# Kernel tuning notes

Measured on AMD Instinct MI355X. Metric: run time of the kernel, lower is better.

## Reference

```python
import jax, jax.numpy as jnp
import numpy as np

N = 100000
IN_DIM, HID_DIM, EMB_DIM = 128, 64, 32
E = 1600000


def _gcn_conv(x, W, b, src, tgt, n):
    """PyG GCNConv: linear transform, add self-loops, sym-normalized scatter-add.
    W: [in, out], b: [out]. src/tgt: [E'] incl. self-loops handled by caller."""
    h = x @ W  # [n, out] -- transform before propagate (PyG order)
    deg = jax.ops.segment_sum(jnp.ones_like(tgt, dtype=h.dtype), tgt, num_segments=n)
    dinv = jnp.where(deg > 0, jax.lax.rsqrt(deg), 0.0)
    norm = dinv[src] * dinv[tgt]  # [E']
    msgs = h[src] * norm[:, None]  # [E', out]
    out = jax.ops.segment_sum(msgs, tgt, num_segments=n)
    return out + b


def setup_inputs() -> dict:
    key = jax.random.key(0)
    ks = jax.random.split(key, 6)
    x = jax.random.normal(ks[0], (N, IN_DIM), dtype=jnp.float32)
    edge_index = jax.random.randint(ks[1], (2, E), 0, N, dtype=jnp.int64)
    s1 = 1.0 / np.sqrt(IN_DIM)
    s2 = 1.0 / np.sqrt(HID_DIM)
    W1 = jax.random.uniform(ks[2], (IN_DIM, HID_DIM), jnp.float32, -s1, s1)
    b1 = jnp.zeros((HID_DIM,), jnp.float32)
    W2 = jax.random.uniform(ks[3], (HID_DIM, EMB_DIM), jnp.float32, -s2, s2)
    b2 = jnp.zeros((EMB_DIM,), jnp.float32)
    return {"x": x, "W1": W1, "b1": b1, "W2": W2, "b2": b2, "edge_index": edge_index}


def reference(x, W1, b1, W2, b2, edge_index):
    n = x.shape[0]
    src, tgt = edge_index[0], edge_index[1]
    # add self-loops once (same graph used by both convs)
    loops = jnp.arange(n, dtype=edge_index.dtype)
    src_sl = jnp.concatenate([src, loops])
    tgt_sl = jnp.concatenate([tgt, loops])
    h = jax.nn.relu(_gcn_conv(x, W1, b1, src_sl, tgt_sl, n))
    z = _gcn_conv(h, W2, b2, src_sl, tgt_sl, n)  # [n, EMB_DIM]
    # decode on original edges: edge-wise dot product
    recon = jnp.sum(z[src] * z[tgt], axis=1)  # [E]
    return z, recon
```

## Files before the change

kernel.cpp:

```cpp
#include <hip/hip_runtime.h>
#include <hip/hip_fp16.h>
#include <math.h>


#define NBMAX 512
#define BSHIFT 8
#define BNODES 256
#define CH 16384
#define PTH 512
#define CAPSHIFT 13
#define CAP (1 << CAPSHIFT)

typedef _Float16 half8 __attribute__((ext_vector_type(8)));
typedef float floatx4 __attribute__((ext_vector_type(4)));

static inline int divup(int a, int b) { return (a + b - 1) / b; }

__device__ inline void acc8(__half2* a, float4 v) {
    const __half2* h = (const __half2*)&v;
    a[0] = __hadd2(a[0], h[0]);
    a[1] = __hadd2(a[1], h[1]);
    a[2] = __hadd2(a[2], h[2]);
    a[3] = __hadd2(a[3], h[3]);
}
__device__ inline unsigned short f2bf(float f) {
    unsigned u = __builtin_bit_cast(unsigned, f);
    u = (u + 0x7FFFu + ((u >> 16) & 1u)) >> 16;
    return (unsigned short)u;
}


__global__ void k_init(int* __restrict__ gcur, unsigned* __restrict__ hs_pad,
                       unsigned* __restrict__ zs_pad) {
    int t = threadIdx.x;
    for (int b = t; b < NBMAX; b += 256) gcur[b] = b << CAPSHIFT;
    if (t < 32) hs_pad[t] = 0;
    else if (t < 48) zs_pad[t - 32] = 0;
}


__global__ __launch_bounds__(PTH) void k_part(const int* __restrict__ src,
                                              const int* __restrict__ tgt,
                                              int* __restrict__ gcur,
                                              unsigned* __restrict__ ebuf, int E, int NB) {
    __shared__ int h[NBMAX];
    __shared__ int base[NBMAX];
    int tid = threadIdx.x;
    int e0 = blockIdx.x * CH;
    for (int b = tid; b < NB; b += PTH) h[b] = 0;
    __syncthreads();
#pragma unroll
    for (int r = 0; r < 8; r++) {
        int e = e0 + (r * PTH + tid) * 4;
        if (e + 3 < E) {
            int4 t4 = *(const int4*)(tgt + e);
            atomicAdd(&h[t4.x >> BSHIFT], 1);
            atomicAdd(&h[t4.y >> BSHIFT], 1);
            atomicAdd(&h[t4.z >> BSHIFT], 1);
            atomicAdd(&h[t4.w >> BSHIFT], 1);
        } else {
            for (int j = 0; j < 4; j++) {
                int ee = e + j;
                if (ee < E) atomicAdd(&h[tgt[ee] >> BSHIFT], 1);
            }
        }
    }
    __syncthreads();
    for (int b = tid; b < NB; b += PTH) {
        int c = h[b];
        base[b] = c ? atomicAdd(&gcur[b], c) : 0;
    }
    __syncthreads();
#pragma unroll
    for (int r = 0; r < 8; r++) {
        int e = e0 + (r * PTH + tid) * 4;
        if (e + 3 < E) {
            int4 t4 = *(const int4*)(tgt + e);
            int4 s4 = *(const int4*)(src + e);
            int tv[4] = {t4.x, t4.y, t4.z, t4.w};
            int sw[4] = {s4.x, s4.y, s4.z, s4.w};
#pragma unroll
            for (int j = 0; j < 4; j++) {
                int t = tv[j];
                int pos = atomicAdd(&base[t >> BSHIFT], 1);
                ebuf[pos] = ((unsigned)(t & (BNODES - 1)) << 23) | (unsigned)sw[j];
            }
        } else {
            for (int j = 0; j < 4; j++) {
                int ee = e + j;
                if (ee < E) {
                    int t = tgt[ee];
                    int pos = atomicAdd(&base[t >> BSHIFT], 1);
                    ebuf[pos] = ((unsigned)(t & (BNODES - 1)) << 23) | (unsigned)src[ee];
                }
            }
        }
    }
}


__global__ __launch_bounds__(256) void k_bfill(const unsigned* __restrict__ ebuf,
                                               const int* __restrict__ gcur,
                                               int* __restrict__ rowbeg,
                                               int* __restrict__ rowend,
                                               int* __restrict__ col,
                                               float* __restrict__ dinv, int n) {
    __shared__ int s_cnt[BNODES];
    __shared__ int s_scan[BNODES];
    __shared__ int s_cur[BNODES];
    int b = blockIdx.x, tid = threadIdx.x;
    int nbase = b << BSHIFT;
    int ebase = b << CAPSHIFT;
    int eend = gcur[b];
    s_cnt[tid] = 0;
    __syncthreads();
    for (int e = ebase + tid; e < eend; e += BNODES) {
        atomicAdd(&s_cnt[ebuf[e] >> 23], 1);
    }
    __syncthreads();
    s_scan[tid] = s_cnt[tid];
    __syncthreads();
    for (int off = 1; off < BNODES; off <<= 1) {
        int t = (tid >= off) ? s_scan[tid - off] : 0;
        __syncthreads();
        s_scan[tid] += t;
        __syncthreads();
    }
    int excl = s_scan[tid] - s_cnt[tid];
    s_cur[tid] = excl;
    int node = nbase + tid;
    if (node < n) {
        rowbeg[node] = ebase + excl;
        rowend[node] = ebase + excl + s_cnt[tid];
        dinv[node] = rsqrtf((float)(s_cnt[tid] + 1));
    }
    __syncthreads();
    for (int e = ebase + tid; e < eend; e += BNODES) {
        unsigned p = ebuf[e];
        int pos = atomicAdd(&s_cur[p >> 23], 1);
        col[ebase + pos] = (int)(p & 0x7FFFFFu);
    }
}


__global__ __launch_bounds__(512) void k_mm1(const float* __restrict__ x,
                                             const float* __restrict__ W1,
                                             const float* __restrict__ dinv,
                                             __half* __restrict__ hs, int n) {
    __shared__ _Float16 Wt[64 * 136];
    int tid = threadIdx.x;
    int nbase = blockIdx.x * 128;
#pragma unroll
    for (int i = 0; i < 8; i++) {
        int f = tid + i * 512;
        int c = f & 63, kp = f >> 6;
        float a = W1[(size_t)(2 * kp) * 64 + c];
        float b = W1[(size_t)(2 * kp + 1) * 64 + c];
        *(__half2*)&Wt[c * 136 + 2 * kp] = __floats2half2_rn(a, b);
    }
    __syncthreads();
    int w = tid >> 6, lane = tid & 63;
    int quad = lane >> 4, m = lane & 15;
    int arow = nbase + w * 16 + m;
    const float* xb = x + (size_t)min(arow, n - 1) * 128;
    floatx4 acc[4] = {{0.f, 0.f, 0.f, 0.f}, {0.f, 0.f, 0.f, 0.f},
                      {0.f, 0.f, 0.f, 0.f}, {0.f, 0.f, 0.f, 0.f}};
#pragma unroll
    for (int kt = 0; kt < 4; kt++) {
        float4 v0 = *(const float4*)(xb + kt * 32 + quad * 8);
        float4 v1 = *(const float4*)(xb + kt * 32 + quad * 8 + 4);
        union { half8 h8; __half2 h2[4]; } ua;
        ua.h2[0] = __floats2half2_rn(v0.x, v0.y);
        ua.h2[1] = __floats2half2_rn(v0.z, v0.w);
        ua.h2[2] = __floats2half2_rn(v1.x, v1.y);
        ua.h2[3] = __floats2half2_rn(v1.z, v1.w);
#pragma unroll
        for (int ct = 0; ct < 4; ct++) {
            half8 b = *(const half8*)&Wt[(ct * 16 + m) * 136 + kt * 32 + quad * 8];
            acc[ct] = __builtin_amdgcn_mfma_f32_16x16x32_f16(ua.h8, b, acc[ct], 0, 0, 0);
        }
    }
#pragma unroll
    for (int reg = 0; reg < 4; reg++) {
        int node = nbase + w * 16 + quad * 4 + reg;
        if (node < n) {
            float d = dinv[node];
#pragma unroll
            for (int ct = 0; ct < 4; ct++) {
                hs[(size_t)node * 64 + ct * 16 + m] = __float2half(acc[ct][reg] * d);
            }
        }
    }
}


__global__ __launch_bounds__(256) void k_conv1(const __half* __restrict__ hs,
                                               const int* __restrict__ rowbeg,
                                               const int* __restrict__ rowend,
                                               const int* __restrict__ col,
                                               const float* __restrict__ dinv,
                                               const float* __restrict__ b1,
                                               __half* __restrict__ h2, int n) {
    int gw = (blockIdx.x * 256 + threadIdx.x) >> 6;
    int lane = threadIdx.x & 63;
    int q = lane >> 4, ln = lane & 15;
    int w = gw * 4 + q;
    if (w >= n) return;
    int qb = q << 4;
    int el = ln >> 3, fl = ln & 7;
    int beg = rowbeg[w], end = rowend[w];
    int deg = end - beg;
    int m = min(16, deg);
    int m2 = min(16, deg - 16);
    int sl = (ln < m) ? col[beg + ln] : 0;
    int sl2 = (ln < m2) ? col[beg + 16 + ln] : 0;
    __half2 a2[4];
#pragma unroll
    for (int j = 0; j < 4; j++) a2[j] = __half2half2(__float2half(0.f));
    int rs = (el == 0) ? w : n;
    float4 S = *(const float4*)(hs + (size_t)rs * 64 + fl * 8);
    float4 L[4];
#pragma unroll
    for (int r = 0; r < 4; r++) {
        int idx = 2 * r + el;
        int s = __shfl(sl, qb + idx);
        int a = (idx < m) ? s : n;
        L[r] = *(const float4*)(hs + (size_t)a * 64 + fl * 8);
    }
    acc8(a2, S);
#pragma unroll
    for (int r = 0; r < 4; r++) acc8(a2, L[r]);
#pragma unroll
    for (int r = 0; r < 4; r++) {
        int idx = 8 + 2 * r + el;
        int s = __shfl(sl, qb + idx);
        int a = (idx < m) ? s : n;
        L[r] = *(const float4*)(hs + (size_t)a * 64 + fl * 8);
    }
#pragma unroll
    for (int r = 0; r < 4; r++) acc8(a2, L[r]);
    if (deg > 16) {
#pragma unroll
        for (int r = 0; r < 4; r++) {
            int idx = 2 * r + el;
            int s = __shfl(sl2, qb + idx);
            int a = (idx < m2) ? s : n;
            L[r] = *(const float4*)(hs + (size_t)a * 64 + fl * 8);
        }
#pragma unroll
        for (int r = 0; r < 4; r++) acc8(a2, L[r]);
#pragma unroll
        for (int r = 0; r < 4; r++) {
            int idx = 8 + 2 * r + el;
            int s = __shfl(sl2, qb + idx);
            int a = (idx < m2) ? s : n;
            L[r] = *(const float4*)(hs + (size_t)a * 64 + fl * 8);
        }
#pragma unroll
        for (int r = 0; r < 4; r++) acc8(a2, L[r]);
    }
    if (deg > 32) {
        for (int b0 = 32; b0 < deg; b0 += 16) {
            int mc = min(16, deg - b0);
            int sl3 = (ln < mc) ? col[beg + b0 + ln] : 0;
            for (int r = 0; r < 8; r++) {
                int idx = 2 * r + el;
                int s = __shfl(sl3, qb + idx);
                int a = (idx < mc) ? s : n;
                float4 v = *(const float4*)(hs + (size_t)a * 64 + fl * 8);
                acc8(a2, v);
            }
        }
    }
    float r[8];
#pragma unroll
    for (int j = 0; j < 4; j++) {
        float2 f = __half22float2(a2[j]);
        r[2 * j] = f.x;
        r[2 * j + 1] = f.y;
    }
#pragma unroll
    for (int j = 0; j < 8; j++) r[j] += __shfl_xor(r[j], 8);

    if (el == 0) {
        float d = dinv[w];
        float4 bb0 = *(const float4*)(b1 + fl * 8);
        float4 bb1 = *(const float4*)(b1 + fl * 8 + 4);
        union { float4 f; __half2 h[4]; } u;
        u.h[0] = __floats2half2_rn(fmaxf(r[0] * d + bb0.x, 0.f),
                                   fmaxf(r[1] * d + bb0.y, 0.f));
        u.h[1] = __floats2half2_rn(fmaxf(r[2] * d + bb0.z, 0.f),
                                   fmaxf(r[3] * d + bb0.w, 0.f));
        u.h[2] = __floats2half2_rn(fmaxf(r[4] * d + bb1.x, 0.f),
                                   fmaxf(r[5] * d + bb1.y, 0.f));
        u.h[3] = __floats2half2_rn(fmaxf(r[6] * d + bb1.z, 0.f),
                                   fmaxf(r[7] * d + bb1.w, 0.f));
        *(float4*)(h2 + (size_t)w * 64 + fl * 8) = u.f;
    }
}


__global__ __launch_bounds__(256) void k_mm2(const __half* __restrict__ h2,
                                             const float* __restrict__ W2,
                                             const float* __restrict__ dinv,
                                             __half* __restrict__ zs, int n) {
    __shared__ _Float16 Wt[32 * 72];
    int tid = threadIdx.x;
    int nbase = blockIdx.x * 64;
#pragma unroll
    for (int i = 0; i < 4; i++) {
        int f = tid + i * 256;
        int c = f & 31, kp = f >> 5;
        float a = W2[(size_t)(2 * kp) * 32 + c];
        float b = W2[(size_t)(2 * kp + 1) * 32 + c];
        *(__half2*)&Wt[c * 72 + 2 * kp] = __floats2half2_rn(a, b);
    }
    __syncthreads();
    int w = tid >> 6, lane = tid & 63;
    int quad = lane >> 4, m = lane & 15;
    int arow = nbase + w * 16 + m;
    const __half* abase = h2 + (size_t)min(arow, n - 1) * 64;
    floatx4 acc[2] = {{0.f, 0.f, 0.f, 0.f}, {0.f, 0.f, 0.f, 0.f}};
#pragma unroll
    for (int kt = 0; kt < 2; kt++) {
        half8 a = *(const half8*)(abase + kt * 32 + quad * 8);
#pragma unroll
        for (int ct = 0; ct < 2; ct++) {
            half8 b = *(const half8*)&Wt[(ct * 16 + m) * 72 + kt * 32 + quad * 8];
            acc[ct] = __builtin_amdgcn_mfma_f32_16x16x32_f16(a, b, acc[ct], 0, 0, 0);
        }
    }
#pragma unroll
    for (int reg = 0; reg < 4; reg++) {
        int node = nbase + w * 16 + quad * 4 + reg;
        if (node < n) {
            float d = dinv[node];
#pragma unroll
            for (int ct = 0; ct < 2; ct++) {
                zs[(size_t)node * 32 + ct * 16 + m] = __float2half(acc[ct][reg] * d);
            }
        }
    }
}


__global__ __launch_bounds__(256) void k_conv2(const __half* __restrict__ zs,
                                               const int* __restrict__ rowbeg,
                                               const int* __restrict__ rowend,
                                               const int* __restrict__ col,
                                               const float* __restrict__ dinv,
                                               const float* __restrict__ b2,
                                               float* __restrict__ zout,
                                               unsigned short* __restrict__ zh, int n) {
    int gw = (blockIdx.x * 256 + threadIdx.x) >> 6;
    int lane = threadIdx.x & 63;
    int q = lane >> 4, ln = lane & 15;
    int w = gw * 4 + q;
    if (w >= n) return;
    int qb = q << 4;
    int el = ln >> 2, fl = ln & 3;
    int beg = rowbeg[w], end = rowend[w];
    int deg = end - beg;
    int m = min(16, deg);
    int m2 = min(16, deg - 16);
    int sl = (ln < m) ? col[beg + ln] : 0;
    int sl2 = (ln < m2) ? col[beg + 16 + ln] : 0;
    __half2 a2[4];
#pragma unroll
    for (int j = 0; j < 4; j++) a2[j] = __half2half2(__float2half(0.f));
    int rs = (el == 0) ? w : n;
    float4 S = *(const float4*)(zs + (size_t)rs * 32 + fl * 8);
    float4 L[4];
#pragma unroll
    for (int r = 0; r < 4; r++) {
        int idx = 4 * r + el;
        int s = __shfl(sl, qb + idx);
        int a = (idx < m) ? s : n;
        L[r] = *(const float4*)(zs + (size_t)a * 32 + fl * 8);
    }
    acc8(a2, S);
#pragma unroll
    for (int r = 0; r < 4; r++) acc8(a2, L[r]);
    if (deg > 16) {
#pragma unroll
        for (int r = 0; r < 4; r++) {
            int idx = 4 * r + el;
            int s = __shfl(sl2, qb + idx);
            int a = (idx < m2) ? s : n;
            L[r] = *(const float4*)(zs + (size_t)a * 32 + fl * 8);
        }
#pragma unroll
        for (int r = 0; r < 4; r++) acc8(a2, L[r]);
    }
    if (deg > 32) {
        for (int b0 = 32; b0 < deg; b0 += 16) {
            int mc = min(16, deg - b0);
            int sl3 = (ln < mc) ? col[beg + b0 + ln] : 0;
            for (int r = 0; r < 4; r++) {
                int idx = 4 * r + el;
                int s = __shfl(sl3, qb + idx);
                int a = (idx < mc) ? s : n;
                float4 v = *(const float4*)(zs + (size_t)a * 32 + fl * 8);
                acc8(a2, v);
            }
        }
    }
    float r[8];
#pragma unroll
    for (int j = 0; j < 4; j++) {
        float2 f = __half22float2(a2[j]);
        r[2 * j] = f.x;
        r[2 * j + 1] = f.y;
    }
#pragma unroll
    for (int d = 4; d < 16; d <<= 1)
#pragma unroll
        for (int j = 0; j < 8; j++) r[j] += __shfl_xor(r[j], d);

    if (el == 0) {
        float d = dinv[w];
        float4 bb0 = *(const float4*)(b2 + fl * 8);
        float4 bb1 = *(const float4*)(b2 + fl * 8 + 4);
        float o0 = r[0] * d + bb0.x, o1 = r[1] * d + bb0.y;
        float o2 = r[2] * d + bb0.z, o3 = r[3] * d + bb0.w;
        float o4 = r[4] * d + bb1.x, o5 = r[5] * d + bb1.y;
        float o6 = r[6] * d + bb1.z, o7 = r[7] * d + bb1.w;
        *(float4*)(zout + (size_t)w * 32 + fl * 8) = make_float4(o0, o1, o2, o3);
        *(float4*)(zout + (size_t)w * 32 + fl * 8 + 4) = make_float4(o4, o5, o6, o7);
        uint4 p;
        p.x = (unsigned)f2bf(o0) | ((unsigned)f2bf(o1) << 16);
        p.y = (unsigned)f2bf(o2) | ((unsigned)f2bf(o3) << 16);
        p.z = (unsigned)f2bf(o4) | ((unsigned)f2bf(o5) << 16);
        p.w = (unsigned)f2bf(o6) | ((unsigned)f2bf(o7) << 16);
        *(uint4*)(zh + (size_t)w * 32 + fl * 8) = p;
    }
}


__device__ inline float bfdot8(uint4 a, uint4 b) {
    const unsigned* pa = (const unsigned*)&a;
    const unsigned* pb = (const unsigned*)&b;
    float v = 0.f;
#pragma unroll
    for (int w = 0; w < 4; w++) {
        float alo = __builtin_bit_cast(float, pa[w] << 16);
        float ahi = __builtin_bit_cast(float, pa[w] & 0xFFFF0000u);
        float blo = __builtin_bit_cast(float, pb[w] << 16);
        float bhi = __builtin_bit_cast(float, pb[w] & 0xFFFF0000u);
        v += alo * blo + ahi * bhi;
    }
    return v;
}

__global__ __launch_bounds__(256) void k_decode(const unsigned short* __restrict__ zh,
                                                const int* __restrict__ src,
                                                const int* __restrict__ tgt,
                                                float* __restrict__ recon, int E) {
    int g = (blockIdx.x * 256 + threadIdx.x) >> 2;
    int fl = threadIdx.x & 3;
    int e0 = g * 4;
    if (e0 >= E) return;
    int cnt = min(4, E - e0);
    int s[4], t[4];
#pragma unroll
    for (int q = 0; q < 4; q++) {
        int e = (q < cnt) ? e0 + q : e0;
        s[q] = src[e];
        t[q] = tgt[e];
    }
    uint4 Za[4], Zb[4];
#pragma unroll
    for (int q = 0; q < 4; q++) {
        Za[q] = *(const uint4*)(zh + (size_t)s[q] * 32 + fl * 8);
        Zb[q] = *(const uint4*)(zh + (size_t)t[q] * 32 + fl * 8);
    }
    float v[4];
#pragma unroll
    for (int q = 0; q < 4; q++) {
        float x = bfdot8(Za[q], Zb[q]);
        x += __shfl_xor(x, 1);
        x += __shfl_xor(x, 2);
        v[q] = x;
    }
    if (fl == 0) {
        if (cnt == 4) {
            *(float4*)(recon + e0) = make_float4(v[0], v[1], v[2], v[3]);
        } else {
            for (int q = 0; q < cnt; q++) recon[e0 + q] = v[q];
        }
    }
}

extern "C" void kernel_launch(void* const* d_in, const int* in_sizes, int n_in,
                              void* d_out, int out_size, void* d_ws, size_t ws_size,
                              hipStream_t stream) {
    const float* x = (const float*)d_in[0];
    const float* W1 = (const float*)d_in[1];
    const float* b1 = (const float*)d_in[2];
    const float* W2 = (const float*)d_in[3];
    const float* b2 = (const float*)d_in[4];
    const int* ei = (const int*)d_in[5];

    int N = in_sizes[0] / 128;
    int E = in_sizes[5] / 2;
    const int* src = ei;
    const int* tgt = ei + E;
    int NB = divup(N, BNODES);

    char* ws = (char*)d_ws;
    size_t off = 0;
    auto alloc = [&](size_t bytes) {
        size_t r = off;
        off += (bytes + 255) & ~(size_t)255;
        return r;
    };
    int* gcur = (int*)(ws + alloc(NBMAX * 4));
    unsigned* ebuf = (unsigned*)(ws + alloc((size_t)NB * CAP * 4));
    int* col = (int*)(ws + alloc((size_t)NB * CAP * 4));
    int* rowbeg = (int*)(ws + alloc((size_t)N * 4));
    int* rowend = (int*)(ws + alloc((size_t)N * 4));
    float* dinv = (float*)(ws + alloc((size_t)N * 4));
    __half* hs = (__half*)(ws + alloc((size_t)(N + 1) * 64 * 2));
    __half* h2 = (__half*)(ws + alloc((size_t)N * 64 * 2));
    __half* zs = (__half*)(ws + alloc((size_t)(N + 1) * 32 * 2));
    unsigned short* zh = (unsigned short*)(ws + alloc((size_t)N * 32 * 2));

    float* zout = (float*)d_out;
    float* recon = zout + (size_t)N * 32;

    k_init<<<1, 256, 0, stream>>>(gcur, (unsigned*)(hs + (size_t)N * 64),
                                  (unsigned*)(zs + (size_t)N * 32));
    k_part<<<divup(E, CH), PTH, 0, stream>>>(src, tgt, gcur, ebuf, E, NB);
    k_bfill<<<NB, BNODES, 0, stream>>>(ebuf, gcur, rowbeg, rowend, col, dinv, N);

    k_mm1<<<divup(N, 128), 512, 0, stream>>>(x, W1, dinv, hs, N);
    k_conv1<<<divup(N, 16), 256, 0, stream>>>(hs, rowbeg, rowend, col, dinv, b1, h2, N);
    k_mm2<<<divup(N, 64), 256, 0, stream>>>(h2, W2, dinv, zs, N);
    k_conv2<<<divup(N, 16), 256, 0, stream>>>(zs, rowbeg, rowend, col, dinv, b2, zout, zh, N);
    k_decode<<<divup(E, 256), 256, 0, stream>>>(zh, src, tgt, recon, E);
}
```

Measured before the change: 226.2 us.

## Fuse all GCN stages into one persistent cooperative kernel with grid syncs

```diff
diff --git a/kernel.cpp b/kernel.cpp
--- a/kernel.cpp
+++ b/kernel.cpp
@@ -1,13 +1,15 @@
 #include <hip/hip_runtime.h>
+#include <hip/hip_cooperative_groups.h>
 #include <hip/hip_fp16.h>
 #include <math.h>
+
+namespace cg = cooperative_groups;
 
 
 #define NBMAX 512
 #define BSHIFT 8
 #define BNODES 256
-#define CH 16384
-#define PTH 512
+#define CHF 16384
 #define CAPSHIFT 13
 #define CAP (1 << CAPSHIFT)
 
@@ -28,6 +30,460 @@
     u = (u + 0x7FFFu + ((u >> 16) & 1u)) >> 16;
     return (unsigned short)u;
 }
+__device__ inline float bfdot8(uint4 a, uint4 b) {
+    const unsigned* pa = (const unsigned*)&a;
+    const unsigned* pb = (const unsigned*)&b;
+    float v = 0.f;
+#pragma unroll
+    for (int w = 0; w < 4; w++) {
+        float alo = __builtin_bit_cast(float, pa[w] << 16);
+        float ahi = __builtin_bit_cast(float, pa[w] & 0xFFFF0000u);
+        float blo = __builtin_bit_cast(float, pb[w] << 16);
+        float bhi = __builtin_bit_cast(float, pb[w] & 0xFFFF0000u);
+        v += alo * blo + ahi * bhi;
+    }
+    return v;
+}
+
+
+struct GP {
+    const float* x; const float* W1; const float* b1;
+    const float* W2; const float* b2;
+    const int* src; const int* tgt;
+    int* gcur; unsigned* ebuf; int* col; int* rowbeg; int* rowend; float* dinv;
+    __half* hs; __half* h2; __half* zs; unsigned short* zh;
+    float* zout; float* recon;
+    int n, e, nb, npart;
+};
+
+__global__ __launch_bounds__(256) void k_fused(GP p) {
+    cg::grid_group grid = cg::this_grid();
+    __shared__ union {
+        struct { int h[NBMAX]; int base[NBMAX]; } pt;
+        struct { int cnt[BNODES]; int scan[BNODES]; int cur[BNODES]; } bf;
+        _Float16 wt1[64 * 136];
+        _Float16 wt2[32 * 72];
+    } sm;
+    const int tid = threadIdx.x;
+    const int nblk = gridDim.x;
+
+    if (blockIdx.x == 0) {
+        for (int b = tid; b < NBMAX; b += 256) p.gcur[b] = b << CAPSHIFT;
+        unsigned* hp = (unsigned*)(p.hs + (size_t)p.n * 64);
+        unsigned* zp = (unsigned*)(p.zs + (size_t)p.n * 32);
+        if (tid < 32) hp[tid] = 0;
+        else if (tid < 48) zp[tid - 32] = 0;
+    }
+    grid.sync();
+
+    for (int vb = blockIdx.x; vb < p.npart; vb += nblk) {
+        __syncthreads();
+        int e0 = vb * CHF;
+        for (int b = tid; b < p.nb; b += 256) sm.pt.h[b] = 0;
+        __syncthreads();
+        for (int r = 0; r < 16; r++) {
+            int e = e0 + (r * 256 + tid) * 4;
+            if (e + 3 < p.e) {
+                int4 t4 = *(const int4*)(p.tgt + e);
+                atomicAdd(&sm.pt.h[t4.x >> BSHIFT], 1);
+                atomicAdd(&sm.pt.h[t4.y >> BSHIFT], 1);
+                atomicAdd(&sm.pt.h[t4.z >> BSHIFT], 1);
+                atomicAdd(&sm.pt.h[t4.w >> BSHIFT], 1);
+            } else {
+                for (int j = 0; j < 4; j++) {
+                    int ee = e + j;
+                    if (ee < p.e) atomicAdd(&sm.pt.h[p.tgt[ee] >> BSHIFT], 1);
+                }
+            }
+        }
+        __syncthreads();
+        for (int b = tid; b < p.nb; b += 256) {
+            int c = sm.pt.h[b];
+            sm.pt.base[b] = c ? atomicAdd(&p.gcur[b], c) : 0;
+        }
+        __syncthreads();
+        for (int r = 0; r < 16; r++) {
+            int e = e0 + (r * 256 + tid) * 4;
+            if (e + 3 < p.e) {
+                int4 t4 = *(const int4*)(p.tgt + e);
+                int4 s4 = *(const int4*)(p.src + e);
+                int tv[4] = {t4.x, t4.y, t4.z, t4.w};
+                int sw[4] = {s4.x, s4.y, s4.z, s4.w};
+#pragma unroll
+                for (int j = 0; j < 4; j++) {
+                    int t = tv[j];
+                    int pos = atomicAdd(&sm.pt.base[t >> BSHIFT], 1);
+                    p.ebuf[pos] = ((unsigned)(t & (BNODES - 1)) << 23) | (unsigned)sw[j];
+                }
+            } else {
+                for (int j = 0; j < 4; j++) {
+                    int ee = e + j;
+                    if (ee < p.e) {
+                        int t = p.tgt[ee];
+                        int pos = atomicAdd(&sm.pt.base[t >> BSHIFT], 1);
+                        p.ebuf[pos] = ((unsigned)(t & (BNODES - 1)) << 23) | (unsigned)p.src[ee];
+                    }
+                }
+            }
+        }
+    }
+    grid.sync();
+
+    for (int vb = blockIdx.x; vb < p.nb; vb += nblk) {
+        __syncthreads();
+        int nbase = vb << BSHIFT;
+        int ebase = vb << CAPSHIFT;
+        int eend = p.gcur[vb];
+        sm.bf.cnt[tid] = 0;
+        __syncthreads();
+        for (int e = ebase + tid; e < eend; e += BNODES) {
+            atomicAdd(&sm.bf.cnt[p.ebuf[e] >> 23], 1);
+        }
+        __syncthreads();
+        sm.bf.scan[tid] = sm.bf.cnt[tid];
+        __syncthreads();
+        for (int off = 1; off < BNODES; off <<= 1) {
+            int t = (tid >= off) ? sm.bf.scan[tid - off] : 0;
+            __syncthreads();
+            sm.bf.scan[tid] += t;
+            __syncthreads();
+        }
+        int excl = sm.bf.scan[tid] - sm.bf.cnt[tid];
+        sm.bf.cur[tid] = excl;
+        int node = nbase + tid;
+        if (node < p.n) {
+            p.rowbeg[node] = ebase + excl;
+            p.rowend[node] = ebase + excl + sm.bf.cnt[tid];
+            p.dinv[node] = rsqrtf((float)(sm.bf.cnt[tid] + 1));
+        }
+        __syncthreads();
+        for (int e = ebase + tid; e < eend; e += BNODES) {
+            unsigned q = p.ebuf[e];
+            int pos = atomicAdd(&sm.bf.cur[q >> 23], 1);
+            p.col[ebase + pos] = (int)(q & 0x7FFFFFu);
+        }
+    }
+    grid.sync();
+
+    {
+#pragma unroll
+        for (int i = 0; i < 16; i++) {
+            int f = tid + i * 256;
+            int c = f & 63, kp = f >> 6;
+            float a = p.W1[(size_t)(2 * kp) * 64 + c];
+            float b = p.W1[(size_t)(2 * kp + 1) * 64 + c];
+            *(__half2*)&sm.wt1[c * 136 + 2 * kp] = __floats2half2_rn(a, b);
+        }
+        __syncthreads();
+        int w = tid >> 6, lane = tid & 63;
+        int quad = lane >> 4, m = lane & 15;
+        int ntile = (p.n + 63) >> 6;
+        for (int vt = blockIdx.x; vt < ntile; vt += nblk) {
+            int nbase = vt * 64;
+            int arow = nbase + w * 16 + m;
+            const float* xb = p.x + (size_t)(arow < p.n ? arow : p.n - 1) * 128;
+            floatx4 acc[4] = {{0.f, 0.f, 0.f, 0.f}, {0.f, 0.f, 0.f, 0.f},
+                              {0.f, 0.f, 0.f, 0.f}, {0.f, 0.f, 0.f, 0.f}};
+#pragma unroll
+            for (int kt = 0; kt < 4; kt++) {
+                float4 v0 = *(const float4*)(xb + kt * 32 + quad * 8);
+                float4 v1 = *(const float4*)(xb + kt * 32 + quad * 8 + 4);
+                union { half8 h8; __half2 h2[4]; } ua;
+                ua.h2[0] = __floats2half2_rn(v0.x, v0.y);
+                ua.h2[1] = __floats2half2_rn(v0.z, v0.w);
+                ua.h2[2] = __floats2half2_rn(v1.x, v1.y);
+                ua.h2[3] = __floats2half2_rn(v1.z, v1.w);
+#pragma unroll
+                for (int ct = 0; ct < 4; ct++) {
+                    half8 b = *(const half8*)&sm.wt1[(ct * 16 + m) * 136 + kt * 32 + quad * 8];
+                    acc[ct] = __builtin_amdgcn_mfma_f32_16x16x32_f16(ua.h8, b, acc[ct], 0, 0, 0);
+                }
+            }
+#pragma unroll
+            for (int reg = 0; reg < 4; reg++) {
+                int node = nbase + w * 16 + quad * 4 + reg;
+                if (node < p.n) {
+                    float d = p.dinv[node];
+#pragma unroll
+                    for (int ct = 0; ct < 4; ct++) {
+                        p.hs[(size_t)node * 64 + ct * 16 + m] = __float2half(acc[ct][reg] * d);
+                    }
+                }
+            }
+        }
+    }
+    grid.sync();
+
+    {
+        int wid = (blockIdx.x * 256 + tid) >> 6;
+        int wstride = (nblk * 256) >> 6;
+        int lane = tid & 63;
+        int q = lane >> 4, ln = lane & 15, qb = q << 4;
+        int el = ln >> 3, fl = ln & 7;
+        for (int gw = wid; gw * 4 < p.n; gw += wstride) {
+            int w = gw * 4 + q;
+            if (w < p.n) {
+                int beg = p.rowbeg[w], end = p.rowend[w];
+                int deg = end - beg;
+                int m = min(16, deg);
+                int m2 = min(16, deg - 16);
+                int sl = (ln < m) ? p.col[beg + ln] : 0;
+                int sl2 = (ln < m2) ? p.col[beg + 16 + ln] : 0;
+                __half2 a2[4];
+#pragma unroll
+                for (int j = 0; j < 4; j++) a2[j] = __half2half2(__float2half(0.f));
+                int rs = (el == 0) ? w : p.n;
+                float4 S = *(const float4*)(p.hs + (size_t)rs * 64 + fl * 8);
+                float4 L[4];
+#pragma unroll
+                for (int r = 0; r < 4; r++) {
+                    int idx = 2 * r + el;
+                    int s = __shfl(sl, qb + idx);
+                    int a = (idx < m) ? s : p.n;
+                    L[r] = *(const float4*)(p.hs + (size_t)a * 64 + fl * 8);
+                }
+                acc8(a2, S);
+#pragma unroll
+                for (int r = 0; r < 4; r++) acc8(a2, L[r]);
+#pragma unroll
+                for (int r = 0; r < 4; r++) {
+                    int idx = 8 + 2 * r + el;
+                    int s = __shfl(sl, qb + idx);
+                    int a = (idx < m) ? s : p.n;
+                    L[r] = *(const float4*)(p.hs + (size_t)a * 64 + fl * 8);
+                }
+#pragma unroll
+                for (int r = 0; r < 4; r++) acc8(a2, L[r]);
+                if (deg > 16) {
+#pragma unroll
+                    for (int r = 0; r < 4; r++) {
+                        int idx = 2 * r + el;
+                        int s = __shfl(sl2, qb + idx);
+                        int a = (idx < m2) ? s : p.n;
+                        L[r] = *(const float4*)(p.hs + (size_t)a * 64 + fl * 8);
+                    }
+#pragma unroll
+                    for (int r = 0; r < 4; r++) acc8(a2, L[r]);
+#pragma unroll
+                    for (int r = 0; r < 4; r++) {
+                        int idx = 8 + 2 * r + el;
+                        int s = __shfl(sl2, qb + idx);
+                        int a = (idx < m2) ? s : p.n;
+                        L[r] = *(const float4*)(p.hs + (size_t)a * 64 + fl * 8);
+                    }
+#pragma unroll
+                    for (int r = 0; r < 4; r++) acc8(a2, L[r]);
+                }
+                if (deg > 32) {
+                    for (int b0 = 32; b0 < deg; b0 += 16) {
+                        int mc = min(16, deg - b0);
+                        int sl3 = (ln < mc) ? p.col[beg + b0 + ln] : 0;
+                        for (int r = 0; r < 8; r++) {
+                            int idx = 2 * r + el;
+                            int s = __shfl(sl3, qb + idx);
+                            int a = (idx < mc) ? s : p.n;
+                            float4 v = *(const float4*)(p.hs + (size_t)a * 64 + fl * 8);
+                            acc8(a2, v);
+                        }
+                    }
+                }
+                float r[8];
+#pragma unroll
+                for (int j = 0; j < 4; j++) {
+                    float2 f = __half22float2(a2[j]);
+                    r[2 * j] = f.x;
+                    r[2 * j + 1] = f.y;
+                }
+#pragma unroll
+                for (int j = 0; j < 8; j++) r[j] += __shfl_xor(r[j], 8);
+                if (el == 0) {
+                    float d = p.dinv[w];
+                    float4 bb0 = *(const float4*)(p.b1 + fl * 8);
+                    float4 bb1 = *(const float4*)(p.b1 + fl * 8 + 4);
+                    union { float4 f; __half2 h[4]; } u;
+                    u.h[0] = __floats2half2_rn(fmaxf(r[0] * d + bb0.x, 0.f),
+                                               fmaxf(r[1] * d + bb0.y, 0.f));
+                    u.h[1] = __floats2half2_rn(fmaxf(r[2] * d + bb0.z, 0.f),
+                                               fmaxf(r[3] * d + bb0.w, 0.f));
+                    u.h[2] = __floats2half2_rn(fmaxf(r[4] * d + bb1.x, 0.f),
+                                               fmaxf(r[5] * d + bb1.y, 0.f));
+                    u.h[3] = __floats2half2_rn(fmaxf(r[6] * d + bb1.z, 0.f),
+                                               fmaxf(r[7] * d + bb1.w, 0.f));
+                    *(float4*)(p.h2 + (size_t)w * 64 + fl * 8) = u.f;
+                }
+            }
+        }
+    }
+    grid.sync();
+
+    {
+#pragma unroll
+        for (int i = 0; i < 4; i++) {
+            int f = tid + i * 256;
+            int c = f & 31, kp = f >> 5;
+            float a = p.W2[(size_t)(2 * kp) * 32 + c];
+            float b = p.W2[(size_t)(2 * kp + 1) * 32 + c];
+            *(__half2*)&sm.wt2[c * 72 + 2 * kp] = __floats2half2_rn(a, b);
+        }
+        __syncthreads();
+        int w = tid >> 6, lane = tid & 63;
+        int quad = lane >> 4, m = lane & 15;
+        int ntile = (p.n + 63) >> 6;
+        for (int vt = blockIdx.x; vt < ntile; vt += nblk) {
+            int nbase = vt * 64;
+            int arow = nbase + w * 16 + m;
+            const __half* abase = p.h2 + (size_t)(arow < p.n ? arow : p.n - 1) * 64;
+            floatx4 acc[2] = {{0.f, 0.f, 0.f, 0.f}, {0.f, 0.f, 0.f, 0.f}};
+#pragma unroll
+            for (int kt = 0; kt < 2; kt++) {
+                half8 a = *(const half8*)(abase + kt * 32 + quad * 8);
+#pragma unroll
+                for (int ct = 0; ct < 2; ct++) {
+                    half8 b = *(const half8*)&sm.wt2[(ct * 16 + m) * 72 + kt * 32 + quad * 8];
+                    acc[ct] = __builtin_amdgcn_mfma_f32_16x16x32_f16(a, b, acc[ct], 0, 0, 0);
+                }
+            }
+#pragma unroll
+            for (int reg = 0; reg < 4; reg++) {
+                int node = nbase + w * 16 + quad * 4 + reg;
+                if (node < p.n) {
+                    float d = p.dinv[node];
+#pragma unroll
+                    for (int ct = 0; ct < 2; ct++) {
+                        p.zs[(size_t)node * 32 + ct * 16 + m] = __float2half(acc[ct][reg] * d);
+                    }
+                }
+            }
+        }
+    }
+    grid.sync();
+
+    {
+        int wid = (blockIdx.x * 256 + tid) >> 6;
+        int wstride = (nblk * 256) >> 6;
+        int lane = tid & 63;
+        int q = lane >> 4, ln = lane & 15, qb = q << 4;
+        int el = ln >> 2, fl = ln & 3;
+        for (int gw = wid; gw * 4 < p.n; gw += wstride) {
+            int w = gw * 4 + q;
+            if (w < p.n) {
+                int beg = p.rowbeg[w], end = p.rowend[w];
+                int deg = end - beg;
+                int m = min(16, deg);
+                int m2 = min(16, deg - 16);
+                int sl = (ln < m) ? p.col[beg + ln] : 0;
+                int sl2 = (ln < m2) ? p.col[beg + 16 + ln] : 0;
+                __half2 a2[4];
+#pragma unroll
+                for (int j = 0; j < 4; j++) a2[j] = __half2half2(__float2half(0.f));
+                int rs = (el == 0) ? w : p.n;
+                float4 S = *(const float4*)(p.zs + (size_t)rs * 32 + fl * 8);
+                float4 L[4];
+#pragma unroll
+                for (int r = 0; r < 4; r++) {
+                    int idx = 4 * r + el;
+                    int s = __shfl(sl, qb + idx);
+                    int a = (idx < m) ? s : p.n;
+                    L[r] = *(const float4*)(p.zs + (size_t)a * 32 + fl * 8);
+                }
+                acc8(a2, S);
+#pragma unroll
+                for (int r = 0; r < 4; r++) acc8(a2, L[r]);
+                if (deg > 16) {
+#pragma unroll
+                    for (int r = 0; r < 4; r++) {
+                        int idx = 4 * r + el;
+                        int s = __shfl(sl2, qb + idx);
+                        int a = (idx < m2) ? s : p.n;
+                        L[r] = *(const float4*)(p.zs + (size_t)a * 32 + fl * 8);
+                    }
+#pragma unroll
+                    for (int r = 0; r < 4; r++) acc8(a2, L[r]);
+                }
+                if (deg > 32) {
+                    for (int b0 = 32; b0 < deg; b0 += 16) {
+                        int mc = min(16, deg - b0);
+                        int sl3 = (ln < mc) ? p.col[beg + b0 + ln] : 0;
+                        for (int r = 0; r < 4; r++) {
+                            int idx = 4 * r + el;
+                            int s = __shfl(sl3, qb + idx);
+                            int a = (idx < mc) ? s : p.n;
+                            float4 v = *(const float4*)(p.zs + (size_t)a * 32 + fl * 8);
+                            acc8(a2, v);
+                        }
+                    }
+                }
+                float r[8];
+#pragma unroll
+                for (int j = 0; j < 4; j++) {
+                    float2 f = __half22float2(a2[j]);
+                    r[2 * j] = f.x;
+                    r[2 * j + 1] = f.y;
+                }
+#pragma unroll
+                for (int d = 4; d < 16; d <<= 1)
+#pragma unroll
+                    for (int j = 0; j < 8; j++) r[j] += __shfl_xor(r[j], d);
+                if (el == 0) {
+                    float d = p.dinv[w];
+                    float4 bb0 = *(const float4*)(p.b2 + fl * 8);
+                    float4 bb1 = *(const float4*)(p.b2 + fl * 8 + 4);
+                    float o0 = r[0] * d + bb0.x, o1 = r[1] * d + bb0.y;
+                    float o2 = r[2] * d + bb0.z, o3 = r[3] * d + bb0.w;
+                    float o4 = r[4] * d + bb1.x, o5 = r[5] * d + bb1.y;
+                    float o6 = r[6] * d + bb1.z, o7 = r[7] * d + bb1.w;
+                    *(float4*)(p.zout + (size_t)w * 32 + fl * 8) = make_float4(o0, o1, o2, o3);
+                    *(float4*)(p.zout + (size_t)w * 32 + fl * 8 + 4) = make_float4(o4, o5, o6, o7);
+                    uint4 pk;
+                    pk.x = (unsigned)f2bf(o0) | ((unsigned)f2bf(o1) << 16);
+                    pk.y = (unsigned)f2bf(o2) | ((unsigned)f2bf(o3) << 16);
+                    pk.z = (unsigned)f2bf(o4) | ((unsigned)f2bf(o5) << 16);
+                    pk.w = (unsigned)f2bf(o6) | ((unsigned)f2bf(o7) << 16);
+                    *(uint4*)(p.zh + (size_t)w * 32 + fl * 8) = pk;
+                }
+            }
+        }
+    }
+    grid.sync();
+
+    {
+        int g = (blockIdx.x * 256 + tid) >> 2;
+        int gstride = nblk * 64;
+        int fl = tid & 3;
+        for (; g * 4 < p.e; g += gstride) {
+            int e0 = g * 4;
+            int cnt = min(4, p.e - e0);
+            int s[4], t[4];
+#pragma unroll
+            for (int q = 0; q < 4; q++) {
+                int e = (q < cnt) ? e0 + q : e0;
+                s[q] = p.src[e];
+                t[q] = p.tgt[e];
+            }
+            uint4 Za[4], Zb[4];
+#pragma unroll
+            for (int q = 0; q < 4; q++) {
+                Za[q] = *(const uint4*)(p.zh + (size_t)s[q] * 32 + fl * 8);
+                Zb[q] = *(const uint4*)(p.zh + (size_t)t[q] * 32 + fl * 8);
+            }
+            float v[4];
+#pragma unroll
+            for (int q = 0; q < 4; q++) {
+                float xv = bfdot8(Za[q], Zb[q]);
+                xv += __shfl_xor(xv, 1);
+                xv += __shfl_xor(xv, 2);
+                v[q] = xv;
+            }
+            if (fl == 0) {
+                if (cnt == 4) {
+                    *(float4*)(p.recon + e0) = make_float4(v[0], v[1], v[2], v[3]);
+                } else {
+                    for (int q = 0; q < cnt; q++) p.recon[e0 + q] = v[q];
+                }
+            }
+        }
+    }
+}
 
 
 __global__ void k_init(int* __restrict__ gcur, unsigned* __restrict__ hs_pad,
@@ -38,20 +494,19 @@
     else if (t < 48) zs_pad[t - 32] = 0;
 }
 
-
-__global__ __launch_bounds__(PTH) void k_part(const int* __restrict__ src,
+__global__ __launch_bounds__(512) void k_part(const int* __restrict__ src,
                                               const int* __restrict__ tgt,
                                               int* __restrict__ gcur,
                                               unsigned* __restrict__ ebuf, int E, int NB) {
     __shared__ int h[NBMAX];
     __shared__ int base[NBMAX];
     int tid = threadIdx.x;
-    int e0 = blockIdx.x * CH;
-    for (int b = tid; b < NB; b += PTH) h[b] = 0;
+    int e0 = blockIdx.x * CHF;
+    for (int b = tid; b < NB; b += 512) h[b] = 0;
     __syncthreads();
 #pragma unroll
     for (int r = 0; r < 8; r++) {
-        int e = e0 + (r * PTH + tid) * 4;
+        int e = e0 + (r * 512 + tid) * 4;
         if (e + 3 < E) {
             int4 t4 = *(const int4*)(tgt + e);
             atomicAdd(&h[t4.x >> BSHIFT], 1);
@@ -66,14 +521,14 @@
         }
     }
     __syncthreads();
-    for (int b = tid; b < NB; b += PTH) {
+    for (int b = tid; b < NB; b += 512) {
         int c = h[b];
         base[b] = c ? atomicAdd(&gcur[b], c) : 0;
     }
     __syncthreads();
 #pragma unroll
     for (int r = 0; r < 8; r++) {
-        int e = e0 + (r * PTH + tid) * 4;
+        int e = e0 + (r * 512 + tid) * 4;
         if (e + 3 < E) {
             int4 t4 = *(const int4*)(tgt + e);
             int4 s4 = *(const int4*)(src + e);
@@ -97,7 +552,6 @@
         }
     }
 }
-
 
 __global__ __launch_bounds__(256) void k_bfill(const unsigned* __restrict__ ebuf,
                                                const int* __restrict__ gcur,
@@ -142,7 +596,6 @@
     }
 }
 
-
 __global__ __launch_bounds__(512) void k_mm1(const float* __restrict__ x,
                                              const float* __restrict__ W1,
                                              const float* __restrict__ dinv,
@@ -192,7 +645,6 @@
         }
     }
 }
-
 
 __global__ __launch_bounds__(256) void k_conv1(const __half* __restrict__ hs,
                                                const int* __restrict__ rowbeg,
@@ -281,7 +733,6 @@
     }
 #pragma unroll
     for (int j = 0; j < 8; j++) r[j] += __shfl_xor(r[j], 8);
-
     if (el == 0) {
         float d = dinv[w];
         float4 bb0 = *(const float4*)(b1 + fl * 8);
@@ -299,7 +750,6 @@
     }
 }
 
-
 __global__ __launch_bounds__(256) void k_mm2(const __half* __restrict__ h2,
                                              const float* __restrict__ W2,
                                              const float* __restrict__ dinv,
@@ -342,7 +792,6 @@
         }
     }
 }
-
 
 __global__ __launch_bounds__(256) void k_conv2(const __half* __restrict__ zs,
                                                const int* __restrict__ rowbeg,
@@ -416,7 +865,6 @@
     for (int d = 4; d < 16; d <<= 1)
 #pragma unroll
         for (int j = 0; j < 8; j++) r[j] += __shfl_xor(r[j], d);
-
     if (el == 0) {
         float d = dinv[w];
         float4 bb0 = *(const float4*)(b2 + fl * 8);
@@ -436,22 +884,6 @@
     }
 }
 
-
-__device__ inline float bfdot8(uint4 a, uint4 b) {
-    const unsigned* pa = (const unsigned*)&a;
-    const unsigned* pb = (const unsigned*)&b;
-    float v = 0.f;
-#pragma unroll
-    for (int w = 0; w < 4; w++) {
-        float alo = __builtin_bit_cast(float, pa[w] << 16);
-        float ahi = __builtin_bit_cast(float, pa[w] & 0xFFFF0000u);
-        float blo = __builtin_bit_cast(float, pb[w] << 16);
-        float bhi = __builtin_bit_cast(float, pb[w] & 0xFFFF0000u);
-        v += alo * blo + ahi * bhi;
-    }
-    return v;
-}
-
 __global__ __launch_bounds__(256) void k_decode(const unsigned short* __restrict__ zh,
                                                 const int* __restrict__ src,
                                                 const int* __restrict__ tgt,
@@ -490,6 +922,7 @@
         }
     }
 }
+
 
 extern "C" void kernel_launch(void* const* d_in, const int* in_sizes, int n_in,
                               void* d_out, int out_size, void* d_ws, size_t ws_size,
@@ -528,14 +961,40 @@
     float* zout = (float*)d_out;
     float* recon = zout + (size_t)N * 32;
 
-    k_init<<<1, 256, 0, stream>>>(gcur, (unsigned*)(hs + (size_t)N * 64),
-                                  (unsigned*)(zs + (size_t)N * 32));
-    k_part<<<divup(E, CH), PTH, 0, stream>>>(src, tgt, gcur, ebuf, E, NB);
-    k_bfill<<<NB, BNODES, 0, stream>>>(ebuf, gcur, rowbeg, rowend, col, dinv, N);
-
-    k_mm1<<<divup(N, 128), 512, 0, stream>>>(x, W1, dinv, hs, N);
-    k_conv1<<<divup(N, 16), 256, 0, stream>>>(hs, rowbeg, rowend, col, dinv, b1, h2, N);
-    k_mm2<<<divup(N, 64), 256, 0, stream>>>(h2, W2, dinv, zs, N);
-    k_conv2<<<divup(N, 16), 256, 0, stream>>>(zs, rowbeg, rowend, col, dinv, b2, zout, zh, N);
-    k_decode<<<divup(E, 256), 256, 0, stream>>>(zh, src, tgt, recon, E);
-}
+    static int s_grid = 0;
+    if (s_grid == 0) {
+        hipDeviceProp_t prop;
+        if (hipGetDeviceProperties(&prop, 0) != hipSuccess) prop.multiProcessorCount = 256;
+        int m = 0;
+        if (hipOccupancyMaxActiveBlocksPerMultiprocessor(&m, k_fused, 256, 0) != hipSuccess || m < 1)
+            m = 1;
+        long g = (long)m * (long)prop.multiProcessorCount;
+        if (g > 2048) g = 2048;
+        if (g < 1) g = 1;
+        s_grid = (int)g;
+    }
+
+    GP p;
+    p.x = x; p.W1 = W1; p.b1 = b1; p.W2 = W2; p.b2 = b2;
+    p.src = src; p.tgt = tgt;
+    p.gcur = gcur; p.ebuf = ebuf; p.col = col;
+    p.rowbeg = rowbeg; p.rowend = rowend; p.dinv = dinv;
+    p.hs = hs; p.h2 = h2; p.zs = zs; p.zh = zh;
+    p.zout = zout; p.recon = recon;
+    p.n = N; p.e = E; p.nb = NB; p.npart = divup(E, CHF);
+
+    void* args[] = {(void*)&p};
+    hipError_t err = hipLaunchCooperativeKernel((const void*)k_fused, dim3(s_grid),
+                                                dim3(256), args, 0, stream);
+    if (err != hipSuccess) {
+        k_init<<<1, 256, 0, stream>>>(gcur, (unsigned*)(hs + (size_t)N * 64),
+                                      (unsigned*)(zs + (size_t)N * 32));
+        k_part<<<divup(E, CHF), 512, 0, stream>>>(src, tgt, gcur, ebuf, E, NB);
+        k_bfill<<<NB, BNODES, 0, stream>>>(ebuf, gcur, rowbeg, rowend, col, dinv, N);
+        k_mm1<<<divup(N, 128), 512, 0, stream>>>(x, W1, dinv, hs, N);
+        k_conv1<<<divup(N, 16), 256, 0, stream>>>(hs, rowbeg, rowend, col, dinv, b1, h2, N);
+        k_mm2<<<divup(N, 64), 256, 0, stream>>>(h2, W2, dinv, zs, N);
+        k_conv2<<<divup(N, 16), 256, 0, stream>>>(zs, rowbeg, rowend, col, dinv, b2, zout, zh, N);
+        k_decode<<<divup(E, 256), 256, 0, stream>>>(zh, src, tgt, recon, E);
+    }
+}
```

After: 662.7 us. 193% more time.
